# Optimization experiments

Measured on AMD Instinct MI355X. Metric: run time of the kernel, lower is better.

## Reference

```python
import jax, jax.numpy as jnp
import numpy as np

B, C, N, T = 8, 32, 4000, 12
KT = 3
TS = 6          # tem_size
SUP_ORD_CH = (2 * 3 + 1) * C  # (order*support_len+1)*c_in = 224
EPS = 1e-5


def setup_inputs() -> dict:
    key = jax.random.key(0)
    ks = jax.random.split(key, 20)
    inp = {
        "x": jax.random.normal(ks[0], (B, C, N, T), dtype=jnp.float32),
        # dense normalized supports (scaled uniform, like row-normalized adjacency)
        "A0": jax.random.uniform(ks[1], (N, N), dtype=jnp.float32) / N,
        "A1": jax.random.uniform(ks[2], (N, N), dtype=jnp.float32) / N,
        "A2": jax.random.uniform(ks[3], (N, N), dtype=jnp.float32) / N,
        # conv1: 1x1 Conv2d(32 -> 32), bias
        "conv1_w": jax.random.normal(ks[4], (C, C), dtype=jnp.float32) * 0.05,
        "conv1_b": jnp.zeros((C,), dtype=jnp.float32),
        # multigcn mlp: Conv2d(224 -> 64, kernel (1, Kt)), bias
        "mlp_w": jax.random.normal(ks[5], (2 * C, SUP_ORD_CH, 1, KT), dtype=jnp.float32) * 0.02,
        "mlp_b": jnp.zeros((2 * C,), dtype=jnp.float32),
        # conv_temp1: 1x1 Conv2d over time axis (10 -> 6), bias
        "ct1_w": jax.random.normal(ks[6], (TS, T - KT + 1), dtype=jnp.float32) * 0.1,
        "ct1_b": jnp.zeros((TS,), dtype=jnp.float32),
        # TATT_1 params
        "tat_c1_w": jax.random.normal(ks[7], (C,), dtype=jnp.float32) * 0.1,   # Conv2d(c_in->1,1x1,no bias)
        "tat_c2_w": jax.random.normal(ks[8], (N,), dtype=jnp.float32) * 0.01,  # Conv2d(N->1,1x1,no bias)
        "tat_w": jax.random.normal(ks[9], (N, C), dtype=jnp.float32) * 0.01,
        "tat_bias": jnp.zeros((TS, TS), dtype=jnp.float32),
        "tat_v": jax.random.normal(ks[10], (TS, TS), dtype=jnp.float32) * 0.3,
        "bn1_g": jnp.ones((TS,), dtype=jnp.float32),
        "bn1_b": jnp.zeros((TS,), dtype=jnp.float32),
        # final BatchNorm2d(c_out)
        "bn2_g": jnp.ones((C,), dtype=jnp.float32),
        "bn2_b": jnp.zeros((C,), dtype=jnp.float32),
    }
    return inp


def reference(x, A0, A1, A2, conv1_w, conv1_b, mlp_w, mlp_b, ct1_w, ct1_b,
              tat_c1_w, tat_c2_w, tat_w, tat_bias, tat_v, bn1_g, bn1_b,
              bn2_g, bn2_b):
    # residual = conv1(x)  (1x1 conv over channels)
    residual = jnp.einsum('oc,bcnl->bonl', conv1_w, x) + conv1_b[None, :, None, None]

    # multi_gcn_time: nconv does A<-A.T then einsum('ncvl,vw->ncwl'),
    # i.e. out[..,w,..] = sum_v x[..,v,..] * A[w,v]
    outs = [x]
    for A in (A0, A1, A2):
        x1 = jnp.einsum('bcvl,wv->bcwl', x, A)
        outs.append(x1)
        x2 = jnp.einsum('bcvl,wv->bcwl', x1, A)
        outs.append(x2)
    h = jnp.concatenate(outs, axis=1)  # (B, 224, N, T)
    h = jax.lax.conv_general_dilated(
        h, mlp_w, window_strides=(1, 1), padding='VALID',
        dimension_numbers=('NCHW', 'OIHW', 'NCHW')) + mlp_b[None, :, None, None]  # (B,64,N,10)

    # gated tanh * sigmoid
    x1, x2 = jnp.split(h, 2, axis=1)
    g = jnp.tanh(x1) * jax.nn.sigmoid(x2)  # (B,32,N,10)

    # conv_temp1: 1x1 conv over the TIME axis (10 -> 6)
    g = jnp.einsum('ql,bcnl->bcnq', ct1_w, g) + ct1_b[None, None, None, :]  # (B,32,N,6)

    # TATT_1 temporal attention coefficients
    f1 = jnp.einsum('c,bcnt->btn', tat_c1_w, g)                       # (B,6,N)
    f2 = jnp.einsum('n,bcnt->bct', tat_c2_w, g)                       # (B,32,6)
    logits = jax.nn.sigmoid(jnp.einsum('btn,nc,bcs->bts', f1, tat_w, f2) + tat_bias)
    logits = jnp.einsum('ts,bsq->btq', tat_v, logits)                 # (B,6,6)
    # BatchNorm1d(tem_size) applied after permute(0,2,1): channel = q axis
    lp = jnp.transpose(logits, (0, 2, 1))
    mu = lp.mean(axis=(0, 2), keepdims=True)
    var = lp.var(axis=(0, 2), keepdims=True)
    lp = (lp - mu) / jnp.sqrt(var + EPS) * bn1_g[None, :, None] + bn1_b[None, :, None]
    logits = jnp.transpose(lp, (0, 2, 1))
    coefs = jax.nn.softmax(logits, axis=-1)                           # (B,6,6)

    # x = einsum('bcnl,blq->bcnq', x, T_coef.transpose(-1,-2))
    Tc = jnp.transpose(coefs, (0, 2, 1))
    out = jnp.einsum('bcnl,blq->bcnq', g, Tc)                         # (B,32,N,6)

    y = out + residual[:, :, :, -out.shape[3]:]
    # BatchNorm2d(c_out), training-mode batch stats
    mu2 = y.mean(axis=(0, 2, 3), keepdims=True)
    var2 = y.var(axis=(0, 2, 3), keepdims=True)
    return (y - mu2) / jnp.sqrt(var2 + EPS) * bn2_g[None, :, None, None] + bn2_b[None, :, None, None]
```

## Files before the change

kernel.cpp:

```cpp
#include <hip/hip_runtime.h>
#include <hip/hip_bf16.h>
#include <cstdint>
#include <cstddef>


typedef __attribute__((ext_vector_type(8))) short s16x8;
typedef __attribute__((ext_vector_type(4))) short s16x4;
typedef __attribute__((ext_vector_type(4))) float f32x4;

#define DEVFN __device__ __forceinline__

DEVFN void gload16(const void* g, void* l) {
  __builtin_amdgcn_global_load_lds((const __attribute__((address_space(1))) unsigned int*)g,
                                   (__attribute__((address_space(3))) unsigned int*)l, 16, 0, 0);
}

DEVFN unsigned short f2bf(float f) {
  union { float f; unsigned int u; } v; v.f = f;
  unsigned int u = v.u;
  return (unsigned short)((u + 0x7fffu + ((u >> 16) & 1u)) >> 16);
}

__global__ void k_transpose(const float* __restrict__ x,
                            unsigned short* __restrict__ Xt,
                            unsigned short* __restrict__ Scat) {
  __shared__ float ldsT[32 * 417];
  int v0 = blockIdx.x * 32;
  int b = blockIdx.y;
  int tid = threadIdx.x;
  for (int i = tid; i < 1024; i += 256) {
    int c = i >> 5, vv = i & 31;
    const float* src = x + ((size_t)(b * 32 + c) * 4000 + v0 + vv) * 12;
    f32x4 a0 = *(const f32x4*)(src);
    f32x4 a1 = *(const f32x4*)(src + 4);
    f32x4 a2 = *(const f32x4*)(src + 8);
    float* d = ldsT + c * 417 + vv * 13;
    d[0] = a0.x; d[1] = a0.y; d[2] = a0.z; d[3] = a0.w;
    d[4] = a1.x; d[5] = a1.y; d[6] = a1.z; d[7] = a1.w;
    d[8] = a2.x; d[9] = a2.y; d[10] = a2.z; d[11] = a2.w;
  }
  __syncthreads();
  for (int unit = tid; unit < 384; unit += 256) {
    int l = unit >> 5, c = unit & 31;
    alignas(16) unsigned short tmp[32];
#pragma unroll
    for (int vv = 0; vv < 32; ++vv) tmp[vv] = f2bf(ldsT[c * 417 + vv * 13 + l]);
    unsigned short* dst = Xt + (size_t)(b * 384 + l * 32 + c) * 4096 + v0;
#pragma unroll
    for (int j = 0; j < 4; ++j) *(s16x8*)(dst + j * 8) = *(const s16x8*)(tmp + j * 8);
  }
  for (int unit = tid; unit < 384; unit += 256) {
    int l = unit >> 5, vv = unit & 31;
    alignas(16) unsigned short tmp[32];
#pragma unroll
    for (int c = 0; c < 32; ++c) tmp[c] = f2bf(ldsT[c * 417 + vv * 13 + l]);
    unsigned short* dst = Scat + ((size_t)(b * 4000 + v0 + vv) * 12 + l) * 224;
#pragma unroll
    for (int j = 0; j < 4; ++j) *(s16x8*)(dst + j * 8) = *(const s16x8*)(tmp + j * 8);
  }
}

__global__ void k_castA(const float* __restrict__ A, unsigned short* __restrict__ Abf) {
  int idx = blockIdx.x * 256 + threadIdx.x;
  int r = idx >> 10;
  int c4 = (idx & 1023) << 2;
  alignas(8) unsigned short o[4] = {0, 0, 0, 0};
  if (r < 4000 && c4 < 4000) {
    f32x4 v = *(const f32x4*)(A + (size_t)r * 4000 + c4);
    o[0] = f2bf(v.x); o[1] = f2bf(v.y); o[2] = f2bf(v.z); o[3] = f2bf(v.w);
  }
  *(s16x4*)(Abf + (size_t)r * 4096 + c4) = *(const s16x4*)o;
}

__global__ void k_wcat(const float* __restrict__ mlp_w, unsigned short* __restrict__ Wcat) {
  int i = blockIdx.x * 256 + threadIdx.x;
  if (i >= 64 * 672) return;
  int oc = i / 672, k = i % 672;
  int kt = k / 224, ic = k % 224;
  Wcat[i] = f2bf(mlp_w[((size_t)oc * 224 + ic) * 3 + kt]);
}

#define MFMA_(a, b, c) __builtin_amdgcn_mfma_f32_16x16x32_bf16(a, b, c, 0, 0, 0)

#define STG(OPER, d, h, t) do {                                                  \
    const unsigned short* _s = (OPER ? baseB : baseA) + (size_t)(h) * 524288 + (size_t)(t) * 64; \
    int _l = (OPER ? 32768 : 0) + ((d) * 2 + (h)) * 8192;                        \
    gload16(_s, smem + _l + tid * 8);                                            \
    gload16(_s + 262144, smem + _l + (512 + tid) * 8);                           \
  } while (0)

#define LDA_(d, mr, kk) (*(const s16x8*)(smem + ((d) * 2 + ha) * 8192 + aoff + (mr) * 1024 + ((kk) ? sxor : 0)))
#define LDB_(d, nr, kk) (*(const s16x8*)(smem + 32768 + ((d) * 2 + hb) * 8192 + boff + (nr) * 1024 + ((kk) ? sxor : 0)))

#define PHASE(d, mp, FIRST, STAGE_CODE, VM) do {                                 \
    s16x8 a00 = LDA_(d, 2 * (mp), 0),     a01 = LDA_(d, 2 * (mp), 1);            \
    s16x8 a10 = LDA_(d, 2 * (mp) + 1, 0), a11 = LDA_(d, 2 * (mp) + 1, 1);        \
    if (FIRST) {                                                                 \
      _Pragma("unroll")                                                          \
      for (int nr = 0; nr < 4; ++nr) { bfr[nr][0] = LDB_(d, nr, 0); bfr[nr][1] = LDB_(d, nr, 1); } \
    }                                                                            \
    STAGE_CODE;                                                                  \
    if (VM) asm volatile("s_waitcnt vmcnt(4)" ::: "memory");                     \
    __builtin_amdgcn_s_barrier();                                                \
    asm volatile("s_waitcnt lgkmcnt(0)" ::: "memory");                           \
    __builtin_amdgcn_s_setprio(1);                                               \
    _Pragma("unroll")                                                            \
    for (int nr = 0; nr < 4; ++nr) {                                             \
      acc[2 * (mp)][nr]     = MFMA_(a00, bfr[nr][0], acc[2 * (mp)][nr]);         \
      acc[2 * (mp)][nr]     = MFMA_(a01, bfr[nr][1], acc[2 * (mp)][nr]);         \
      acc[2 * (mp) + 1][nr] = MFMA_(a10, bfr[nr][0], acc[2 * (mp) + 1][nr]);     \
      acc[2 * (mp) + 1][nr] = MFMA_(a11, bfr[nr][1], acc[2 * (mp) + 1][nr]);     \
    }                                                                            \
    __builtin_amdgcn_s_setprio(0);                                               \
    __builtin_amdgcn_s_barrier();                                                \
  } while (0)

template <int MODE>
__global__ __launch_bounds__(512, 2)
void k_gemm(const unsigned short* __restrict__ P, const unsigned short* __restrict__ Q,
            unsigned short* __restrict__ C1, unsigned short* __restrict__ Scat, int jcol) {
  extern __shared__ unsigned short smem[];
  int tid = threadIdx.x;
  int w = tid >> 6, lane = tid & 63;
  int lr = lane & 15, g = lane >> 4;
  int bid = blockIdx.x;
  int xcd = bid & 7, lid = bid >> 3;
  int mt, nt;
  if (MODE == 0) { mt = (xcd & 3) * 3 + (lid >> 3); nt = (xcd >> 2) * 8 + (lid & 7); }
  else           { nt = (xcd & 3) * 3 + (lid >> 3); mt = (xcd >> 2) * 8 + (lid & 7); }
  int m0 = mt * 256, n0 = nt * 256;
  int ha = w >> 2;
  int hb = (w & 3) >> 1;
  int wn = (w & 3) * 64;
  int slot0 = (g ^ (lr & 7)) * 8;
  int aoff = lr * 64 + slot0;
  int boff = ((w & 1) * 64 + lr) * 64 + slot0;
  int sxor = (slot0 & 32) ? -32 : 32;
  int gk = ((tid & 7) ^ ((tid >> 3) & 7)) * 8;
  const unsigned short* baseA = P + (size_t)(m0 + (tid >> 3)) * 4096 + gk;
  const unsigned short* baseB = Q + (size_t)(n0 + (tid >> 3)) * 4096 + gk;
  f32x4 acc[8][4] = {};
  s16x8 bfr[4][2];

  STG(1, 0, 0, 0); STG(1, 0, 1, 0);
  STG(0, 0, 0, 0); STG(0, 0, 1, 0);
  STG(1, 1, 0, 1); STG(1, 1, 1, 1);
  asm volatile("s_waitcnt vmcnt(4)" ::: "memory");
  __builtin_amdgcn_s_barrier();

#pragma unroll 1
  for (int i = 0; i < 32; ++i) {
    int t1 = 2 * i + 1, t2 = 2 * i + 2, t3 = 2 * i + 3;
    PHASE(0, 0, 1, STG(0, 1, 0, t1), 0);
    PHASE(0, 1, 0, STG(0, 1, 1, t1), 0);
    PHASE(0, 2, 0, STG(1, 0, 0, t2), 0);
    PHASE(0, 3, 0, STG(1, 0, 1, t2), 1);
    PHASE(1, 0, 1, STG(0, 0, 0, t2), 0);
    PHASE(1, 1, 0, STG(0, 0, 1, t2), 0);
    PHASE(1, 2, 0, STG(1, 1, 0, t3), 0);
    PHASE(1, 3, 0, STG(1, 1, 1, t3), 1);
  }

  asm volatile("s_waitcnt vmcnt(0) lgkmcnt(0)" ::: "memory");
  __syncthreads();
  unsigned short* eld = smem;
  int rb = g * 4;
#pragma unroll
  for (int h = 0; h < 2; ++h) {
    if (h) __syncthreads();
    if ((w >> 2) == h) {
#pragma unroll
      for (int mr = 0; mr < 8; ++mr)
#pragma unroll
        for (int nr = 0; nr < 4; ++nr)
#pragma unroll
          for (int r = 0; r < 4; ++r)
            eld[(mr * 16 + rb + r) * 264 + wn + nr * 16 + lr] = f2bf(acc[mr][nr][r]);
    }
    __syncthreads();
    if (MODE == 0) {
      int rowh = tid >> 2, q = tid & 3;
      unsigned short* dst = C1 + (size_t)(m0 + h * 128 + rowh) * 4096 + n0 + q * 64;
      const unsigned short* sp = eld + rowh * 264 + q * 64;
#pragma unroll
      for (int j = 0; j < 8; ++j) *(s16x8*)(dst + j * 8) = *(const s16x8*)(sp + j * 8);
#pragma unroll
      for (int uu = 0; uu < 2; ++uu) {
        int u = uu * 512 + tid;
        int lg = u >> 8, nl = u & 255;
        int node = n0 + nl;
        if (node < 4000) {
          int gcol = m0 + h * 128 + lg * 32;
          int bb2 = gcol / 384, ll = (gcol % 384) >> 5;
          alignas(16) unsigned short tmp[32];
#pragma unroll
          for (int c = 0; c < 32; ++c) tmp[c] = eld[(lg * 32 + c) * 264 + nl];
          unsigned short* d2 = Scat + ((size_t)(bb2 * 4000 + node) * 12 + ll) * 224 + jcol;
#pragma unroll
          for (int j = 0; j < 4; ++j) *(s16x8*)(d2 + j * 8) = *(const s16x8*)(tmp + j * 8);
        }
      }
    } else {
#pragma unroll
      for (int uu = 0; uu < 2; ++uu) {
        int u = uu * 512 + tid;
        int lg = u >> 7, nrow = u & 127;
        int node = m0 + h * 128 + nrow;
        if (node < 4000) {
          int gcol = n0 + lg * 32;
          int bb2 = gcol / 384, ll = (gcol % 384) >> 5;
          alignas(16) unsigned short tmp[32];
          const unsigned short* sp = eld + nrow * 264 + lg * 32;
#pragma unroll
          for (int j = 0; j < 4; ++j) *(s16x8*)(tmp + j * 8) = *(const s16x8*)(sp + j * 8);
          unsigned short* d2 = Scat + ((size_t)(bb2 * 4000 + node) * 12 + ll) * 224 + jcol;
#pragma unroll
          for (int j = 0; j < 4; ++j) *(s16x8*)(d2 + j * 8) = *(const s16x8*)(tmp + j * 8);
        }
      }
    }
  }
}

__global__ __launch_bounds__(256, 2)
void k_mlp(const unsigned short* __restrict__ Wcat, const unsigned short* __restrict__ Scat,
           const float* __restrict__ mlp_b, float* __restrict__ G) {
  __shared__ unsigned short lds[2048 + 8192];
  unsigned short* Ws = lds;
  unsigned short* Bs = lds + 2048;
  int tid = threadIdx.x;
  int bn0 = blockIdx.x * 256;
  int t = blockIdx.y;
  int w = tid >> 6, lane = tid & 63;
  int lr = lane & 15, lk = (lane >> 4) * 8;
  f32x4 acc[4][4] = {};
  const unsigned short* gw = Wcat + (size_t)(tid >> 2) * 672 + (tid & 3) * 8;
  const unsigned short* gq = Scat + ((size_t)(bn0 + (tid >> 2)) * 12 + t) * 224 + (tid & 3) * 8;
  unsigned short* lw = Ws + tid * 8;
  unsigned short* lq = Bs + tid * 8;
  for (int s = 0; s < 21; ++s) {
    gload16(gw + s * 32, lw);
#pragma unroll
    for (int r = 0; r < 4; ++r)
      gload16(gq + (size_t)r * 64 * 2688 + s * 32, lq + r * 2048);
    __syncthreads();
    s16x8 a[4], bb[4];
#pragma unroll
    for (int f = 0; f < 4; ++f) {
      a[f] = *(const s16x8*)(Ws + (f * 16 + lr) * 32 + lk);
      bb[f] = *(const s16x8*)(Bs + (w * 64 + f * 16 + lr) * 32 + lk);
    }
#pragma unroll
    for (int fm = 0; fm < 4; ++fm)
#pragma unroll
      for (int fn = 0; fn < 4; ++fn)
        acc[fm][fn] = __builtin_amdgcn_mfma_f32_16x16x32_bf16(a[fm], bb[fn], acc[fm][fn], 0, 0, 0);
    __syncthreads();
  }
  int rbase = (lane >> 4) * 4;
#pragma unroll
  for (int fn = 0; fn < 4; ++fn) {
    int bn = bn0 + w * 64 + fn * 16 + lr;
    int b = bn / 4000;
    int n = bn - b * 4000;
    float* gbase = G + (size_t)(b * 10 + t) * 32 * 4096 + n;
#pragma unroll
    for (int fm = 0; fm < 2; ++fm)
#pragma unroll
      for (int r = 0; r < 4; ++r) {
        int c = fm * 16 + rbase + r;
        float v1 = acc[fm][fn][r] + mlp_b[c];
        float v2 = acc[fm + 2][fn][r] + mlp_b[c + 32];
        gbase[(size_t)c * 4096] = tanhf(v1) * (1.0f / (1.0f + __expf(-v2)));
      }
  }
}

__global__ void k_ct1(const float* __restrict__ G, const float* __restrict__ ct1_w,
                      const float* __restrict__ ct1_b, float* __restrict__ g6) {
  int idx = blockIdx.x * 256 + threadIdx.x;
  if (idx >= 8 * 32 * 4000) return;
  int n = idx % 4000;
  int c = (idx / 4000) % 32;
  int b = idx / (4000 * 32);
  const float* gp = G + ((size_t)(b * 10) * 32 + c) * 4096 + n;
  float v[10];
#pragma unroll
  for (int l = 0; l < 10; ++l) v[l] = gp[(size_t)l * 32 * 4096];
  float* o = g6 + (size_t)idx * 6;
#pragma unroll
  for (int q = 0; q < 6; ++q) {
    float a = ct1_b[q];
#pragma unroll
    for (int l = 0; l < 10; ++l) a += ct1_w[q * 10 + l] * v[l];
    o[q] = a;
  }
}

__global__ void k_f1(const float* __restrict__ g6, const float* __restrict__ c1,
                     float* __restrict__ f1) {
  int idx = blockIdx.x * 128 + threadIdx.x;
  if (idx >= 8 * 4000) return;
  int n = idx % 4000, b = idx / 4000;
  float acc[6] = {};
  const float* gp = g6 + ((size_t)b * 32 * 4000 + n) * 6;
  for (int c = 0; c < 32; ++c) {
    float wv = c1[c];
    const float* p = gp + (size_t)c * 4000 * 6;
#pragma unroll
    for (int t = 0; t < 6; ++t) acc[t] += wv * p[t];
  }
  for (int t = 0; t < 6; ++t) f1[((size_t)b * 6 + t) * 4000 + n] = acc[t];
}

__global__ void k_f2(const float* __restrict__ g6, const float* __restrict__ c2,
                     float* __restrict__ f2) {
  __shared__ float red[256 * 6];
  int bc = blockIdx.x;
  int tid = threadIdx.x;
  float acc[6] = {};
  const float* gp = g6 + (size_t)bc * 4000 * 6;
  for (int n = tid; n < 4000; n += 256) {
    float wv = c2[n];
#pragma unroll
    for (int t = 0; t < 6; ++t) acc[t] += wv * gp[(size_t)n * 6 + t];
  }
  for (int t = 0; t < 6; ++t) red[tid * 6 + t] = acc[t];
  __syncthreads();
  for (int s = 128; s > 0; s >>= 1) {
    if (tid < s)
      for (int t = 0; t < 6; ++t) red[tid * 6 + t] += red[(tid + s) * 6 + t];
    __syncthreads();
  }
  if (tid < 6) f2[bc * 6 + tid] = red[tid];
}

__global__ void k_m1(const float* __restrict__ f1, const float* __restrict__ tw,
                     float* __restrict__ m1) {
  __shared__ float red[8][32];
  int bt = blockIdx.x;
  int nc = blockIdx.y;
  int tid = threadIdx.x;
  int c = tid & 31, gi = tid >> 5;
  float acc = 0.f;
  const float* fp = f1 + (size_t)bt * 4000 + nc * 250;
  const float* twp = tw + ((size_t)nc * 250) * 32 + c;
  for (int n = gi; n < 250; n += 8) acc += fp[n] * twp[n * 32];
  red[gi][c] = acc;
  __syncthreads();
  if (tid < 32) {
    float s = 0.f;
#pragma unroll
    for (int gg = 0; gg < 8; ++gg) s += red[gg][c];
    atomicAdd(&m1[(size_t)bt * 32 + c], s);
  }
}

__global__ void k_att(const float* __restrict__ m1, const float* __restrict__ f2,
                      const float* __restrict__ bias, const float* __restrict__ tv,
                      const float* __restrict__ g1, const float* __restrict__ b1,
                      float* __restrict__ coefs) {
  __shared__ float sig[48 * 6], lgs[48 * 6], mu[6], iv[6];
  int tid = threadIdx.x;
  int b = tid / 6, t = tid % 6;
  if (tid < 48) {
    for (int s = 0; s < 6; ++s) {
      float a = bias[t * 6 + s];
      for (int c = 0; c < 32; ++c)
        a += m1[((size_t)b * 6 + t) * 32 + c] * f2[((size_t)b * 32 + c) * 6 + s];
      sig[tid * 6 + s] = 1.0f / (1.0f + __expf(-a));
    }
  }
  __syncthreads();
  if (tid < 48) {
    for (int q = 0; q < 6; ++q) {
      float a = 0.f;
      for (int s = 0; s < 6; ++s) a += tv[t * 6 + s] * sig[(b * 6 + s) * 6 + q];
      lgs[tid * 6 + q] = a;
    }
  }
  __syncthreads();
  if (tid < 6) {
    float s = 0, s2 = 0;
    for (int r = 0; r < 48; ++r) { float v = lgs[r * 6 + tid]; s += v; s2 += v * v; }
    float m = s / 48.f;
    mu[tid] = m;
    iv[tid] = rsqrtf(s2 / 48.f - m * m + 1e-5f);
  }
  __syncthreads();
  if (tid < 48) {
    float v[6], mx = -1e30f;
    for (int q = 0; q < 6; ++q) {
      v[q] = (lgs[tid * 6 + q] - mu[q]) * iv[q] * g1[q] + b1[q];
      mx = fmaxf(mx, v[q]);
    }
    float s = 0;
    for (int q = 0; q < 6; ++q) { v[q] = __expf(v[q] - mx); s += v[q]; }
    float inv = 1.0f / s;
    for (int q = 0; q < 6; ++q) coefs[tid * 6 + q] = v[q] * inv;
  }
}

__global__ void k_final1(const float* __restrict__ x, const float* __restrict__ cw,
                         const float* __restrict__ cb, const float* __restrict__ g6,
                         const float* __restrict__ coefs, float* __restrict__ out) {
  __shared__ float xt[32 * 8 * 6];
  __shared__ float cwT[1024];
  __shared__ float cfs[36], cbs[32];
  int n0 = blockIdx.x * 8;
  int b = blockIdx.y;
  int tid = threadIdx.x;
  {
    int ci = tid >> 3, seg = tid & 7;
    const float* xp = x + ((size_t)(b * 32 + ci) * 4000 + n0 + seg) * 12 + 6;
#pragma unroll
    for (int q = 0; q < 6; ++q) xt[(ci * 8 + seg) * 6 + q] = xp[q];
  }
  for (int i = tid; i < 1024; i += 256) { int o = i >> 5, ci = i & 31; cwT[ci * 32 + o] = cw[i]; }
  if (tid < 36) cfs[tid] = coefs[b * 36 + tid];
  if (tid < 32) cbs[tid] = cb[tid];
  __syncthreads();
  int nn = tid & 7, c = tid >> 3;
  const float* gp = g6 + ((size_t)(b * 32 + c) * 4000 + n0 + nn) * 6;
  float gv[6];
#pragma unroll
  for (int l = 0; l < 6; ++l) gv[l] = gp[l];
  float y[6];
#pragma unroll
  for (int q = 0; q < 6; ++q) {
    float at = 0.f;
#pragma unroll
    for (int l = 0; l < 6; ++l) at += gv[l] * cfs[q * 6 + l];
    y[q] = at + cbs[c];
  }
  for (int ci = 0; ci < 32; ++ci) {
    float wv = cwT[ci * 32 + c];
#pragma unroll
    for (int q = 0; q < 6; ++q) y[q] += wv * xt[(ci * 8 + nn) * 6 + q];
  }
  float* op = out + ((size_t)(b * 32 + c) * 4000 + n0 + nn) * 6;
#pragma unroll
  for (int q = 0; q < 6; ++q) op[q] = y[q];
}

__global__ void k_stats(const float* __restrict__ out, float* __restrict__ stats) {
  __shared__ float r1[4], r2[4];
  int bc = blockIdx.y;
  int c = bc & 31;
  int tid = threadIdx.x;
  const float* p = out + (size_t)bc * 24000 + blockIdx.x * 6000;
  float s = 0.f, s2 = 0.f;
  for (int i = tid * 4; i < 6000; i += 1024) {
    f32x4 v = *(const f32x4*)(p + i);
    s  += v.x + v.y + v.z + v.w;
    s2 += v.x * v.x + v.y * v.y + v.z * v.z + v.w * v.w;
  }
#pragma unroll
  for (int off = 32; off > 0; off >>= 1) {
    s  += __shfl_down(s, off);
    s2 += __shfl_down(s2, off);
  }
  int lane = tid & 63, w = tid >> 6;
  if (lane == 0) { r1[w] = s; r2[w] = s2; }
  __syncthreads();
  if (tid == 0) {
    atomicAdd(&stats[c],      r1[0] + r1[1] + r1[2] + r1[3]);
    atomicAdd(&stats[32 + c], r2[0] + r2[1] + r2[2] + r2[3]);
  }
}

__global__ void k_final2(float* __restrict__ out, const float* __restrict__ stats,
                         const float* __restrict__ g2, const float* __restrict__ b2) {
  int idx = (blockIdx.x * 256 + threadIdx.x) * 4;
  if (idx >= 6144000) return;
  int c = (idx / 24000) % 32;
  float mean = stats[c] * (1.0f / 192000.f);
  float var = stats[32 + c] * (1.0f / 192000.f) - mean * mean;
  float sc = rsqrtf(var + 1e-5f) * g2[c];
  float sh = b2[c] - mean * sc;
  f32x4 v = *(f32x4*)(out + idx);
  v.x = v.x * sc + sh; v.y = v.y * sc + sh; v.z = v.z * sc + sh; v.w = v.w * sc + sh;
  *(f32x4*)(out + idx) = v;
}

extern "C" void kernel_launch(void* const* d_in, const int* in_sizes, int n_in,
                              void* d_out, int out_size, void* d_ws, size_t ws_size,
                              hipStream_t stream) {
  (void)in_sizes; (void)n_in; (void)out_size;
  const float* x       = (const float*)d_in[0];
  const float* A[3]    = {(const float*)d_in[1], (const float*)d_in[2], (const float*)d_in[3]};
  const float* conv1_w = (const float*)d_in[4];
  const float* conv1_b = (const float*)d_in[5];
  const float* mlp_w   = (const float*)d_in[6];
  const float* mlp_b   = (const float*)d_in[7];
  const float* ct1_w   = (const float*)d_in[8];
  const float* ct1_b   = (const float*)d_in[9];
  const float* c1w     = (const float*)d_in[10];
  const float* c2w     = (const float*)d_in[11];
  const float* tw      = (const float*)d_in[12];
  const float* tbias   = (const float*)d_in[13];
  const float* tv      = (const float*)d_in[14];
  const float* bn1g    = (const float*)d_in[15];
  const float* bn1b    = (const float*)d_in[16];
  const float* bn2g    = (const float*)d_in[17];
  const float* bn2b    = (const float*)d_in[18];
  float* out = (float*)d_out;

  char* ws = (char*)d_ws;
  size_t off = 0;
  auto alloc = [&](size_t bytes) { size_t r = off; off += (bytes + 255) & ~(size_t)255; return r; };
  size_t oScat = alloc(172032000);
  size_t oXt   = alloc(25165824);
  size_t oA    = alloc(33554432);
  size_t oY1t  = alloc(25165824);
  size_t oWcat = alloc(86016);
  size_t oF1 = alloc(768000);
  size_t oF2 = alloc(6144);
  size_t oM1 = alloc(6144);
  size_t oCf = alloc(1152);
  size_t oSt = alloc(256);
  if (ws_size < off) return;

  unsigned short* Scat = (unsigned short*)(ws + oScat);
  unsigned short* Xt   = (unsigned short*)(ws + oXt);
  float*          g6   = (float*)(ws + oXt);
  unsigned short* Abf  = (unsigned short*)(ws + oA);
  float*          G    = (float*)(ws + oA);
  unsigned short* Y1t  = (unsigned short*)(ws + oY1t);
  unsigned short* Wcat = (unsigned short*)(ws + oWcat);

  hipFuncSetAttribute((const void*)k_gemm<0>, hipFuncAttributeMaxDynamicSharedMemorySize, 131072);
  hipFuncSetAttribute((const void*)k_gemm<1>, hipFuncAttributeMaxDynamicSharedMemorySize, 131072);

  hipMemsetAsync(Xt, 0, 25165824, stream);
  hipMemsetAsync(ws + oSt, 0, 256, stream);
  hipMemsetAsync(ws + oM1, 0, 6144, stream);
  k_transpose<<<dim3(125, 8), 256, 0, stream>>>(x, Xt, Scat);
  k_wcat<<<168, 256, 0, stream>>>(mlp_w, Wcat);
  for (int i = 0; i < 3; ++i) {
    k_castA<<<16384, 256, 0, stream>>>(A[i], Abf);
    k_gemm<0><<<192, 512, 131072, stream>>>(Xt, Abf, Y1t, Scat, (2 * i + 1) * 32);
    k_gemm<1><<<192, 512, 131072, stream>>>(Abf, Y1t, nullptr, Scat, (2 * i + 2) * 32);
  }
  k_mlp<<<dim3(125, 10), 256, 0, stream>>>(Wcat, Scat, mlp_b, G);
  k_ct1<<<4000, 256, 0, stream>>>(G, ct1_w, ct1_b, g6);
  k_f1<<<250, 128, 0, stream>>>(g6, c1w, (float*)(ws + oF1));
  k_f2<<<256, 256, 0, stream>>>(g6, c2w, (float*)(ws + oF2));
  k_m1<<<dim3(48, 16), 256, 0, stream>>>((float*)(ws + oF1), tw, (float*)(ws + oM1));
  k_att<<<1, 64, 0, stream>>>((float*)(ws + oM1), (float*)(ws + oF2), tbias, tv, bn1g, bn1b,
                              (float*)(ws + oCf));
  k_final1<<<dim3(500, 8), 256, 0, stream>>>(x, conv1_w, conv1_b, g6, (float*)(ws + oCf), out);
  k_stats<<<dim3(4, 256), 256, 0, stream>>>(out, (float*)(ws + oSt));
  k_final2<<<6000, 256, 0, stream>>>(out, (float*)(ws + oSt), bn2g, bn2b);
}
```

Measured before the change: 909.5 us.

## Retile node GEMMs to 192x256 so 256 blocks fill every CU

The graph-propagation GEMM tile changes from 256x256 to 192x256, with a 3-phase pipeline per k-step, so the grid grows from 192 to 256 blocks, one per compute unit. The second GEMM now computes the transposed product (features x nodes) with the same kernel layout as the first, which lets both share one epilogue that scatters into Scat. LDS use drops to 112 KB. The trade-off is a smaller A tile, so each block reuses the B operand over fewer rows and issues more global loads per MFMA.

```diff
diff --git a/kernel.cpp b/kernel.cpp
--- a/kernel.cpp
+++ b/kernel.cpp
@@ -82,22 +82,30 @@
 
 #define MFMA_(a, b, c) __builtin_amdgcn_mfma_f32_16x16x32_bf16(a, b, c, 0, 0, 0)
 
-#define STG(OPER, d, h, t) do {                                                  \
-    const unsigned short* _s = (OPER ? baseB : baseA) + (size_t)(h) * 524288 + (size_t)(t) * 64; \
-    int _l = (OPER ? 32768 : 0) + ((d) * 2 + (h)) * 8192;                        \
-    gload16(_s, smem + _l + tid * 8);                                            \
-    gload16(_s + 262144, smem + _l + (512 + tid) * 8);                           \
+#define STGA(d, t) do {                                                          \
+    const unsigned short* _s = aSrc + (size_t)(t) * 64;                          \
+    unsigned short* _l = smem + (d) * 12288;                                     \
+    gload16(_s,          _l + tid * 8);                                          \
+    gload16(_s + 262144, _l + (512 + tid) * 8);                                  \
+    gload16(_s + 524288, _l + (1024 + tid) * 8);                                 \
   } while (0)
 
-#define LDA_(d, mr, kk) (*(const s16x8*)(smem + ((d) * 2 + ha) * 8192 + aoff + (mr) * 1024 + ((kk) ? sxor : 0)))
-#define LDB_(d, nr, kk) (*(const s16x8*)(smem + 32768 + ((d) * 2 + hb) * 8192 + boff + (nr) * 1024 + ((kk) ? sxor : 0)))
+#define STGB(d, h, t) do {                                                       \
+    const unsigned short* _s = bSrc + (size_t)(h) * 524288 + (size_t)(t) * 64;   \
+    unsigned short* _l = smem + 24576 + ((d) * 2 + (h)) * 8192;                  \
+    gload16(_s,          _l + tid * 8);                                          \
+    gload16(_s + 262144, _l + (512 + tid) * 8);                                  \
+  } while (0)
+
+#define LDA_(d, f, kk) (*(const s16x8*)(smem + (d) * 12288 + aoff + (f) * 1024 + ((kk) ? sxor : 0)))
+#define LDB_(d, nf, kk) (*(const s16x8*)(smem + 24576 + ((d) * 2 + hb) * 8192 + boff + (nf) * 1024 + ((kk) ? sxor : 0)))
 
 #define PHASE(d, mp, FIRST, STAGE_CODE, VM) do {                                 \
     s16x8 a00 = LDA_(d, 2 * (mp), 0),     a01 = LDA_(d, 2 * (mp), 1);            \
     s16x8 a10 = LDA_(d, 2 * (mp) + 1, 0), a11 = LDA_(d, 2 * (mp) + 1, 1);        \
     if (FIRST) {                                                                 \
       _Pragma("unroll")                                                          \
-      for (int nr = 0; nr < 4; ++nr) { bfr[nr][0] = LDB_(d, nr, 0); bfr[nr][1] = LDB_(d, nr, 1); } \
+      for (int nf = 0; nf < 4; ++nf) { bfr[nf][0] = LDB_(d, nf, 0); bfr[nf][1] = LDB_(d, nf, 1); } \
     }                                                                            \
     STAGE_CODE;                                                                  \
     if (VM) asm volatile("s_waitcnt vmcnt(4)" ::: "memory");                     \
@@ -105,17 +113,17 @@
     asm volatile("s_waitcnt lgkmcnt(0)" ::: "memory");                           \
     __builtin_amdgcn_s_setprio(1);                                               \
     _Pragma("unroll")                                                            \
-    for (int nr = 0; nr < 4; ++nr) {                                             \
-      acc[2 * (mp)][nr]     = MFMA_(a00, bfr[nr][0], acc[2 * (mp)][nr]);         \
-      acc[2 * (mp)][nr]     = MFMA_(a01, bfr[nr][1], acc[2 * (mp)][nr]);         \
-      acc[2 * (mp) + 1][nr] = MFMA_(a10, bfr[nr][0], acc[2 * (mp) + 1][nr]);     \
-      acc[2 * (mp) + 1][nr] = MFMA_(a11, bfr[nr][1], acc[2 * (mp) + 1][nr]);     \
+    for (int nf = 0; nf < 4; ++nf) {                                             \
+      acc[2 * (mp)][nf]     = MFMA_(a00, bfr[nf][0], acc[2 * (mp)][nf]);         \
+      acc[2 * (mp)][nf]     = MFMA_(a01, bfr[nf][1], acc[2 * (mp)][nf]);         \
+      acc[2 * (mp) + 1][nf] = MFMA_(a10, bfr[nf][0], acc[2 * (mp) + 1][nf]);     \
+      acc[2 * (mp) + 1][nf] = MFMA_(a11, bfr[nf][1], acc[2 * (mp) + 1][nf]);     \
     }                                                                            \
     __builtin_amdgcn_s_setprio(0);                                               \
     __builtin_amdgcn_s_barrier();                                                \
   } while (0)
 
-template <int MODE>
+template <int WRITE_C1>
 __global__ __launch_bounds__(512, 2)
 void k_gemm(const unsigned short* __restrict__ P, const unsigned short* __restrict__ Q,
             unsigned short* __restrict__ C1, unsigned short* __restrict__ Scat, int jcol) {
@@ -123,42 +131,39 @@
   int tid = threadIdx.x;
   int w = tid >> 6, lane = tid & 63;
   int lr = lane & 15, g = lane >> 4;
+  int mq = w >> 1, nq = w & 1;
+  mq = w >> 2; nq = w & 3;
   int bid = blockIdx.x;
   int xcd = bid & 7, lid = bid >> 3;
-  int mt, nt;
-  if (MODE == 0) { mt = (xcd & 3) * 3 + (lid >> 3); nt = (xcd >> 2) * 8 + (lid & 7); }
-  else           { nt = (xcd & 3) * 3 + (lid >> 3); mt = (xcd >> 2) * 8 + (lid & 7); }
-  int m0 = mt * 256, n0 = nt * 256;
-  int ha = w >> 2;
-  int hb = (w & 3) >> 1;
-  int wn = (w & 3) * 64;
+  int nt = xcd * 2 + (lid >> 4);
+  int mt = lid & 15;
+  int m0 = mt * 192, n0 = nt * 256;
+  int hb = nq >> 1;
   int slot0 = (g ^ (lr & 7)) * 8;
-  int aoff = lr * 64 + slot0;
-  int boff = ((w & 1) * 64 + lr) * 64 + slot0;
   int sxor = (slot0 & 32) ? -32 : 32;
+  int aoff = (mq * 96 + lr) * 64 + slot0;
+  int boff = ((nq & 1) * 64 + lr) * 64 + slot0;
   int gk = ((tid & 7) ^ ((tid >> 3) & 7)) * 8;
-  const unsigned short* baseA = P + (size_t)(m0 + (tid >> 3)) * 4096 + gk;
-  const unsigned short* baseB = Q + (size_t)(n0 + (tid >> 3)) * 4096 + gk;
-  f32x4 acc[8][4] = {};
+  const unsigned short* aSrc = P + (size_t)(m0 + (tid >> 3)) * 4096 + gk;
+  const unsigned short* bSrc = Q + (size_t)(n0 + (tid >> 3)) * 4096 + gk;
+  f32x4 acc[6][4] = {};
   s16x8 bfr[4][2];
 
-  STG(1, 0, 0, 0); STG(1, 0, 1, 0);
-  STG(0, 0, 0, 0); STG(0, 0, 1, 0);
-  STG(1, 1, 0, 1); STG(1, 1, 1, 1);
+  STGB(0, 0, 0); STGB(0, 1, 0);
+  STGA(0, 0);
+  STGB(1, 0, 1); STGB(1, 1, 1);
   asm volatile("s_waitcnt vmcnt(4)" ::: "memory");
   __builtin_amdgcn_s_barrier();
 
 #pragma unroll 1
   for (int i = 0; i < 32; ++i) {
     int t1 = 2 * i + 1, t2 = 2 * i + 2, t3 = 2 * i + 3;
-    PHASE(0, 0, 1, STG(0, 1, 0, t1), 0);
-    PHASE(0, 1, 0, STG(0, 1, 1, t1), 0);
-    PHASE(0, 2, 0, STG(1, 0, 0, t2), 0);
-    PHASE(0, 3, 0, STG(1, 0, 1, t2), 1);
-    PHASE(1, 0, 1, STG(0, 0, 0, t2), 0);
-    PHASE(1, 1, 0, STG(0, 0, 1, t2), 0);
-    PHASE(1, 2, 0, STG(1, 1, 0, t3), 0);
-    PHASE(1, 3, 0, STG(1, 1, 1, t3), 1);
+    PHASE(0, 0, 1, STGA(1, t1), 0);
+    PHASE(0, 1, 0, STGB(0, 0, t2), 0);
+    PHASE(0, 2, 0, STGB(0, 1, t2), 1);
+    PHASE(1, 0, 1, STGA(0, t2), 0);
+    PHASE(1, 1, 0, STGB(1, 0, t3), 0);
+    PHASE(1, 2, 0, STGB(1, 1, t3), 1);
   }
 
   asm volatile("s_waitcnt vmcnt(0) lgkmcnt(0)" ::: "memory");
@@ -166,58 +171,39 @@
   unsigned short* eld = smem;
   int rb = g * 4;
 #pragma unroll
-  for (int h = 0; h < 2; ++h) {
-    if (h) __syncthreads();
-    if ((w >> 2) == h) {
-#pragma unroll
-      for (int mr = 0; mr < 8; ++mr)
-#pragma unroll
-        for (int nr = 0; nr < 4; ++nr)
-#pragma unroll
-          for (int r = 0; r < 4; ++r)
-            eld[(mr * 16 + rb + r) * 264 + wn + nr * 16 + lr] = f2bf(acc[mr][nr][r]);
+  for (int f = 0; f < 6; ++f)
+#pragma unroll
+    for (int nf = 0; nf < 4; ++nf)
+#pragma unroll
+      for (int r = 0; r < 4; ++r)
+        eld[(mq * 96 + f * 16 + rb + r) * 264 + nq * 64 + nf * 16 + lr] = f2bf(acc[f][nf][r]);
+  __syncthreads();
+  if (WRITE_C1) {
+#pragma unroll
+    for (int uu = 0; uu < 2; ++uu) {
+      int u = uu * 512 + tid;
+      if (u < 768) {
+        int row = u >> 2, q = u & 3;
+        unsigned short* dst = C1 + (size_t)(m0 + row) * 4096 + n0 + q * 64;
+        const unsigned short* sp = eld + row * 264 + q * 64;
+#pragma unroll
+        for (int j = 0; j < 8; ++j) *(s16x8*)(dst + j * 8) = *(const s16x8*)(sp + j * 8);
+      }
     }
-    __syncthreads();
-    if (MODE == 0) {
-      int rowh = tid >> 2, q = tid & 3;
-      unsigned short* dst = C1 + (size_t)(m0 + h * 128 + rowh) * 4096 + n0 + q * 64;
-      const unsigned short* sp = eld + rowh * 264 + q * 64;
-#pragma unroll
-      for (int j = 0; j < 8; ++j) *(s16x8*)(dst + j * 8) = *(const s16x8*)(sp + j * 8);
-#pragma unroll
-      for (int uu = 0; uu < 2; ++uu) {
-        int u = uu * 512 + tid;
-        int lg = u >> 8, nl = u & 255;
-        int node = n0 + nl;
-        if (node < 4000) {
-          int gcol = m0 + h * 128 + lg * 32;
-          int bb2 = gcol / 384, ll = (gcol % 384) >> 5;
-          alignas(16) unsigned short tmp[32];
-#pragma unroll
-          for (int c = 0; c < 32; ++c) tmp[c] = eld[(lg * 32 + c) * 264 + nl];
-          unsigned short* d2 = Scat + ((size_t)(bb2 * 4000 + node) * 12 + ll) * 224 + jcol;
-#pragma unroll
-          for (int j = 0; j < 4; ++j) *(s16x8*)(d2 + j * 8) = *(const s16x8*)(tmp + j * 8);
-        }
-      }
-    } else {
-#pragma unroll
-      for (int uu = 0; uu < 2; ++uu) {
-        int u = uu * 512 + tid;
-        int lg = u >> 7, nrow = u & 127;
-        int node = m0 + h * 128 + nrow;
-        if (node < 4000) {
-          int gcol = n0 + lg * 32;
-          int bb2 = gcol / 384, ll = (gcol % 384) >> 5;
-          alignas(16) unsigned short tmp[32];
-          const unsigned short* sp = eld + nrow * 264 + lg * 32;
-#pragma unroll
-          for (int j = 0; j < 4; ++j) *(s16x8*)(tmp + j * 8) = *(const s16x8*)(sp + j * 8);
-          unsigned short* d2 = Scat + ((size_t)(bb2 * 4000 + node) * 12 + ll) * 224 + jcol;
-#pragma unroll
-          for (int j = 0; j < 4; ++j) *(s16x8*)(d2 + j * 8) = *(const s16x8*)(tmp + j * 8);
-        }
-      }
+  }
+  int bb2 = m0 / 384, lb = (m0 % 384) >> 5;
+#pragma unroll
+  for (int uu = 0; uu < 3; ++uu) {
+    int u = uu * 512 + tid;
+    int lg = u >> 8, nl = u & 255;
+    int node = n0 + nl;
+    if (node < 4000) {
+      alignas(16) unsigned short tmp[32];
+#pragma unroll
+      for (int c = 0; c < 32; ++c) tmp[c] = eld[(lg * 32 + c) * 264 + nl];
+      unsigned short* d2 = Scat + ((size_t)(bb2 * 4000 + node) * 12 + lb + lg) * 224 + jcol;
+#pragma unroll
+      for (int j = 0; j < 4; ++j) *(s16x8*)(d2 + j * 8) = *(const s16x8*)(tmp + j * 8);
     }
   }
 }
@@ -529,8 +515,8 @@
   unsigned short* Y1t  = (unsigned short*)(ws + oY1t);
   unsigned short* Wcat = (unsigned short*)(ws + oWcat);
 
-  hipFuncSetAttribute((const void*)k_gemm<0>, hipFuncAttributeMaxDynamicSharedMemorySize, 131072);
-  hipFuncSetAttribute((const void*)k_gemm<1>, hipFuncAttributeMaxDynamicSharedMemorySize, 131072);
+  hipFuncSetAttribute((const void*)k_gemm<0>, hipFuncAttributeMaxDynamicSharedMemorySize, 114688);
+  hipFuncSetAttribute((const void*)k_gemm<1>, hipFuncAttributeMaxDynamicSharedMemorySize, 114688);
 
   hipMemsetAsync(Xt, 0, 25165824, stream);
   hipMemsetAsync(ws + oSt, 0, 256, stream);
@@ -539,8 +525,8 @@
   k_wcat<<<168, 256, 0, stream>>>(mlp_w, Wcat);
   for (int i = 0; i < 3; ++i) {
     k_castA<<<16384, 256, 0, stream>>>(A[i], Abf);
-    k_gemm<0><<<192, 512, 131072, stream>>>(Xt, Abf, Y1t, Scat, (2 * i + 1) * 32);
-    k_gemm<1><<<192, 512, 131072, stream>>>(Abf, Y1t, nullptr, Scat, (2 * i + 2) * 32);
+    k_gemm<1><<<256, 512, 114688, stream>>>(Xt, Abf, Y1t, Scat, (2 * i + 1) * 32);
+    k_gemm<0><<<256, 512, 114688, stream>>>(Y1t, Abf, nullptr, Scat, (2 * i + 2) * 32);
   }
   k_mlp<<<dim3(125, 10), 256, 0, stream>>>(Wcat, Scat, mlp_b, G);
   k_ct1<<<4000, 256, 0, stream>>>(G, ct1_w, ct1_b, g6);
```

Result: faster. 819.9 us (-9.8%).
